# Optimization experiments

Measured on AMD Instinct MI355X. Metric: run time of the kernel, lower is better.

Reference implementation:

```python
import jax, jax.numpy as jnp
import numpy as np

B, C, H, W = 4, 256, 96, 96
PARA, MOD, NH = 256, 256, 128
PI = 3.14159  # constant used in the torch source (not math.pi)


def setup_inputs():
    key = jax.random.key(0)
    ks = jax.random.split(key, 16)
    w = lambda k, shp: jax.random.normal(k, shp, jnp.float32) * 0.02
    z = lambda n: jnp.zeros((n,), jnp.float32)
    return {
        "feature_map": jax.random.normal(ks[0], (B, C, H, W), jnp.float32),
        "para_code": jax.random.normal(ks[1], (B, PARA), jnp.float32),
        "style_code": jax.random.normal(ks[2], (B, MOD), jnp.float32),
        "lin_common_w": w(ks[3], (PARA, PARA)), "lin_common_b": z(PARA),
        "lin_scale_w": w(ks[4], (PARA, C)), "lin_scale_b": z(C),
        "lin_rot_w": w(ks[5], (PARA, C)), "lin_rot_b": z(C),
        "lin_trans_w": w(ks[6], (PARA, 2 * C)), "lin_trans_b": z(2 * C),
        "a1_shared_w": w(ks[7], (MOD, NH)), "a1_shared_b": z(NH),
        "a1_gamma_w": w(ks[8], (NH, C)), "a1_gamma_b": z(C),
        "a1_beta_w": w(ks[9], (NH, C)), "a1_beta_b": z(C),
        "conv1_w": w(ks[10], (C, C, 3, 3)), "conv1_b": z(C),
        "a2_shared_w": w(ks[11], (MOD, NH)), "a2_shared_b": z(NH),
        "a2_gamma_w": w(ks[12], (NH, C)), "a2_gamma_b": z(C),
        "a2_beta_w": w(ks[13], (NH, C)), "a2_beta_b": z(C),
        "conv2_w": w(ks[14], (C, C, 3, 3)), "conv2_b": z(C),
    }


def _adaat(fm, pc, cw, cb, sw, sb, rw, rb, tw, tb):
    # fm: [B,C,H,W]; per-channel 2D affine warp, channels act as depth of a 3D grid_sample.
    Bn, Cn, Hn, Wn = fm.shape
    pc = jax.nn.relu(pc @ cw + cb)
    scale = jax.nn.sigmoid(pc @ sw + sb) * 2.0            # [B,C]
    angle = jnp.tanh(pc @ rw + rb) * PI                   # [B,C]
    trans = jnp.tanh(pc @ tw + tb).reshape(Bn, Cn, 2)     # [B,C,2]
    cos = jnp.cos(angle)[:, :, None, None]
    sin = jnp.sin(angle)[:, :, None, None]
    sc = scale[:, :, None, None]
    tx = trans[:, :, 0][:, :, None, None]
    ty = trans[:, :, 1][:, :, None, None]
    # align_corners=True style normalized source grid (as in make_coordinate_grid_3d)
    gx = (2.0 * jnp.arange(Wn) / (Wn - 1) - 1.0)[None, :]  # [1,W]
    gy = (2.0 * jnp.arange(Hn) / (Hn - 1) - 1.0)[:, None]  # [H,1]
    # rotation [[cos,-sin],[sin,cos]] @ [x,y], then scale + translate -> [B,C,H,W]
    xw = (cos * gx - sin * gy) * sc + tx
    yw = (sin * gx + cos * gy) * sc + ty
    gz = 2.0 * jnp.arange(Cn) / (Cn - 1) - 1.0             # [C]
    # unnormalize with align_corners=False (torch grid_sample default)
    ix = ((xw + 1.0) * Wn - 1.0) * 0.5
    iy = ((yw + 1.0) * Hn - 1.0) * 0.5
    iz = (((gz + 1.0) * Cn - 1.0) * 0.5)[None, :, None, None]  # [1,C,1,1]
    x0 = jnp.floor(ix); y0 = jnp.floor(iy); z0 = jnp.floor(iz)
    wx = ix - x0; wy = iy - y0; wz = iz - z0
    x0 = x0.astype(jnp.int32); y0 = y0.astype(jnp.int32); z0 = z0.astype(jnp.int32)
    bidx = jnp.arange(Bn)[:, None, None, None]

    def gather(zi, yi, xi):
        valid = (zi >= 0) & (zi < Cn) & (yi >= 0) & (yi < Hn) & (xi >= 0) & (xi < Wn)
        v = fm[bidx, jnp.clip(zi, 0, Cn - 1), jnp.clip(yi, 0, Hn - 1), jnp.clip(xi, 0, Wn - 1)]
        return jnp.where(valid, v, 0.0)

    out = jnp.zeros_like(fm)
    for dz, wzc in ((0, 1.0 - wz), (1, wz)):
        for dy, wyc in ((0, 1.0 - wy), (1, wy)):
            for dx, wxc in ((0, 1.0 - wx), (1, wx)):
                out = out + gather(z0 + dz, y0 + dy, x0 + dx) * (wzc * wyc * wxc)
    return out


def _adain_layer(x, style, shw, shb, gw, gb, bw, bb):
    m = x.mean(axis=(2, 3), keepdims=True)
    v = x.var(axis=(2, 3), keepdims=True)  # biased, as torch InstanceNorm2d
    xn = (x - m) / jnp.sqrt(v + 1e-5)
    a = jax.nn.relu(style @ shw + shb)
    gamma = (a @ gw + gb)[:, :, None, None]
    beta = (a @ bw + bb)[:, :, None, None]
    return xn * (1.0 + gamma) + beta


def _conv3(x, w, b):
    y = jax.lax.conv_general_dilated(x, w, (1, 1), ((1, 1), (1, 1)),
                                     dimension_numbers=("NCHW", "OIHW", "NCHW"))
    return y + b[None, :, None, None]


def _lrelu(x):
    return jnp.where(x >= 0, x, 0.2 * x)


def reference(feature_map, para_code, style_code,
              lin_common_w, lin_common_b, lin_scale_w, lin_scale_b,
              lin_rot_w, lin_rot_b, lin_trans_w, lin_trans_b,
              a1_shared_w, a1_shared_b, a1_gamma_w, a1_gamma_b, a1_beta_w, a1_beta_b,
              conv1_w, conv1_b,
              a2_shared_w, a2_shared_b, a2_gamma_w, a2_gamma_b, a2_beta_w, a2_beta_b,
              conv2_w, conv2_b):
    t = _adaat(feature_map, para_code, lin_common_w, lin_common_b,
               lin_scale_w, lin_scale_b, lin_rot_w, lin_rot_b, lin_trans_w, lin_trans_b)
    x = _adain_layer(t, style_code, a1_shared_w, a1_shared_b, a1_gamma_w, a1_gamma_b, a1_beta_w, a1_beta_b)
    x = _conv3(_lrelu(x), conv1_w, conv1_b)
    x = _adain_layer(x, style_code, a2_shared_w, a2_shared_b, a2_gamma_w, a2_gamma_b, a2_beta_w, a2_beta_b)
    x = _conv3(_lrelu(x), conv2_w, conv2_b)
    return x
```

## Files before the change

### kernel.cpp

```cpp
#include <hip/hip_runtime.h>
#include <hip/hip_bf16.h>
#include <cstddef>

#define BATCH 4
#define CH 256
#define HH 96
#define WW 96
#define HWN (HH*WW)
#define NTOT (BATCH*CH*HWN)
#define XT_H 98
#define XT_W 98
#define XT_PLANE (XT_H*XT_W*CH)

typedef __attribute__((ext_vector_type(16))) float f32x16;
typedef __attribute__((ext_vector_type(8))) __bf16 bfrag;
typedef __attribute__((ext_vector_type(8))) unsigned short u16x8;

static __device__ __forceinline__ unsigned short f2bf(float f) {
  unsigned int u = __float_as_uint(f);
  unsigned int r = (u + 0x7fffu + ((u >> 16) & 1u)) >> 16;
  return (unsigned short)r;
}

__global__ __launch_bounds__(256) void params_kernel(
    const float* __restrict__ para, const float* __restrict__ style,
    const float* __restrict__ cw,  const float* __restrict__ cb,
    const float* __restrict__ sw,  const float* __restrict__ sb,
    const float* __restrict__ rw,  const float* __restrict__ rb,
    const float* __restrict__ tw,  const float* __restrict__ tb,
    const float* __restrict__ a1w, const float* __restrict__ a1b,
    const float* __restrict__ g1w, const float* __restrict__ g1b,
    const float* __restrict__ b1w, const float* __restrict__ b1b,
    const float* __restrict__ a2w, const float* __restrict__ a2b,
    const float* __restrict__ g2w, const float* __restrict__ g2b,
    const float* __restrict__ b2w, const float* __restrict__ b2b,
    float* __restrict__ warp, float* __restrict__ gb1, float* __restrict__ gb2)
{
  __shared__ float s_para[256], s_sty[256], s_pc[256], s_a1[128], s_a2[128];
  int b = blockIdx.x;
  int t = threadIdx.x;
  s_para[t] = para[b*256 + t];
  s_sty[t]  = style[b*256 + t];
  __syncthreads();

  float acc = cb[t];
  for (int i = 0; i < 256; i++) acc = fmaf(s_para[i], cw[i*256 + t], acc);
  s_pc[t] = fmaxf(acc, 0.f);

  if (t < 128) {
    float a = a1b[t];
    for (int i = 0; i < 256; i++) a = fmaf(s_sty[i], a1w[i*128 + t], a);
    s_a1[t] = fmaxf(a, 0.f);
  } else {
    int u = t - 128;
    float a = a2b[u];
    for (int i = 0; i < 256; i++) a = fmaf(s_sty[i], a2w[i*128 + u], a);
    s_a2[u] = fmaxf(a, 0.f);
  }
  __syncthreads();

  int c = t;
  float ds = sb[c], dr = rb[c], dtx = tb[2*c], dty = tb[2*c + 1];
  for (int i = 0; i < 256; i++) {
    float p = s_pc[i];
    ds  = fmaf(p, sw[i*256 + c], ds);
    dr  = fmaf(p, rw[i*256 + c], dr);
    dtx = fmaf(p, tw[i*512 + 2*c], dtx);
    dty = fmaf(p, tw[i*512 + 2*c + 1], dty);
  }
  float scale = 2.f / (1.f + expf(-ds));
  float ang = tanhf(dr) * 3.14159f;
  float sn, cs;
  sincosf(ang, &sn, &cs);
  int bc = b*256 + c;
  warp[bc*4 + 0] = cs * scale;
  warp[bc*4 + 1] = sn * scale;
  warp[bc*4 + 2] = tanhf(dtx);
  warp[bc*4 + 3] = tanhf(dty);

  float g1 = g1b[c], be1 = b1b[c], g2 = g2b[c], be2 = b2b[c];
  for (int i = 0; i < 128; i++) {
    float a = s_a1[i];
    g1  = fmaf(a, g1w[i*256 + c], g1);
    be1 = fmaf(a, b1w[i*256 + c], be1);
  }
  for (int i = 0; i < 128; i++) {
    float a = s_a2[i];
    g2  = fmaf(a, g2w[i*256 + c], g2);
    be2 = fmaf(a, b2w[i*256 + c], be2);
  }
  gb1[bc*2] = g1; gb1[bc*2 + 1] = be1;
  gb2[bc*2] = g2; gb2[bc*2 + 1] = be2;
}

__global__ __launch_bounds__(256) void prep_weights_kernel(
    const float* __restrict__ w1, const float* __restrict__ w2,
    unsigned short* __restrict__ wf1, unsigned short* __restrict__ wf2)
{
  int co = blockIdx.x & 255;
  const float* src = (blockIdx.x < 256) ? w1 : w2;
  unsigned short* dst = (blockIdx.x < 256) ? wf1 : wf2;
  int ci = threadIdx.x;
  int coblk = co >> 6, m = (co >> 5) & 1;
  int l = (co & 31) | (((ci >> 3) & 1) << 5);
  int ks = ci >> 4, j = ci & 7;
  const float* p = src + ((size_t)co * 256 + ci) * 9;
  #pragma unroll
  for (int tap = 0; tap < 9; tap++) {
    size_t idx = (((size_t)((coblk * 16 + ks) * 9 + tap) * 2 + m) * 64 + l) * 8 + j;
    dst[idx] = f2bf(p[tap]);
  }
}

__global__ __launch_bounds__(256) void adaat_kernel(
    const float* __restrict__ fm, const float* __restrict__ warp,
    const float* __restrict__ gb1, float* __restrict__ tout,
    float* __restrict__ nrm1)
{
  __shared__ float s[96 * 100];
  int bc = blockIdx.x;
  int b = bc >> 8, c = bc & 255;
  float csc = warp[bc*4 + 0], ssc = warp[bc*4 + 1];
  float tx = warp[bc*4 + 2], ty = warp[bc*4 + 3];

  const float axw = csc * (96.f / 95.f);
  const float axh = -ssc * (96.f / 95.f);
  const float ax0 = 48.f * (tx - csc + ssc) + 47.5f;
  const float ayw = ssc * (96.f / 95.f);
  const float ayh = csc * (96.f / 95.f);
  const float ay0 = 48.f * (ty - ssc - csc) + 47.5f;

  float iz = 256.f * (float)c / 255.f - 0.5f;
  float z0f = floorf(iz);
  float wz = iz - z0f;
  int z0 = (int)z0f;
  const float* p0 = (z0 >= 0) ? fm + (size_t)(b*256 + z0) * HWN : nullptr;
  const float* p1 = (z0 + 1 < 256) ? fm + (size_t)(b*256 + z0 + 1) * HWN : nullptr;
  float w0 = 1.f - wz, w1 = wz;

  int t = threadIdx.x;
  const float4* q0 = (const float4*)p0;
  const float4* q1 = (const float4*)p1;
  for (int i = t; i < 2304; i += 256) {
    int row = i / 24, col = i - row * 24;
    float4 r = {0.f, 0.f, 0.f, 0.f};
    if (q0) {
      float4 v = q0[i];
      r.x = w0 * v.x; r.y = w0 * v.y; r.z = w0 * v.z; r.w = w0 * v.w;
    }
    if (q1) {
      float4 v = q1[i];
      r.x = fmaf(w1, v.x, r.x); r.y = fmaf(w1, v.y, r.y);
      r.z = fmaf(w1, v.z, r.z); r.w = fmaf(w1, v.w, r.w);
    }
    *(float4*)&s[row * 100 + col * 4] = r;
  }
  __syncthreads();

  int h = t / 96, w = t - (t / 96) * 96;
  float* dst = tout + (size_t)bc * HWN;
  float sum = 0.f, sumsq = 0.f;
  #pragma unroll
  for (int k = 0; k < 36; k++) {
    float ix = fmaf(axw, (float)w, fmaf(axh, (float)h, ax0));
    float iy = fmaf(ayw, (float)w, fmaf(ayh, (float)h, ay0));
    float x0f = floorf(ix), y0f = floorf(iy);
    float wx = ix - x0f, wy = iy - y0f;
    int x0 = (int)x0f, y0 = (int)y0f;
    int x0c = min(max(x0, 0), 95), x1c = min(max(x0 + 1, 0), 95);
    int y0c = min(max(y0, 0), 95), y1c = min(max(y0 + 1, 0), 95);
    bool vx0 = (unsigned)x0 < 96u, vx1 = (unsigned)(x0 + 1) < 96u;
    bool vy0 = (unsigned)y0 < 96u, vy1 = (unsigned)(y0 + 1) < 96u;
    float a00 = s[y0c * 100 + x0c], a01 = s[y0c * 100 + x1c];
    float a10 = s[y1c * 100 + x0c], a11 = s[y1c * 100 + x1c];
    float wxm = 1.f - wx, wym = 1.f - wy;
    float w00 = (vy0 && vx0) ? wym * wxm : 0.f;
    float w01 = (vy0 && vx1) ? wym * wx  : 0.f;
    float w10 = (vy1 && vx0) ? wy * wxm  : 0.f;
    float w11 = (vy1 && vx1) ? wy * wx   : 0.f;
    float v = w00 * a00;
    v = fmaf(w01, a01, v);
    v = fmaf(w10, a10, v);
    v = fmaf(w11, a11, v);
    dst[t + k * 256] = v;
    sum += v;
    sumsq = fmaf(v, v, sumsq);
    int wn = w + 64;
    int carry = (wn >= 96) ? 1 : 0;
    w = wn - (carry ? 96 : 0);
    h += 2 + carry;
  }

  for (int off = 32; off > 0; off >>= 1) {
    sum   += __shfl_down(sum, off, 64);
    sumsq += __shfl_down(sumsq, off, 64);
  }
  __shared__ float rs[4], rq[4];
  int lane = t & 63, wvi = t >> 6;
  if (lane == 0) { rs[wvi] = sum; rq[wvi] = sumsq; }
  __syncthreads();
  if (t == 0) {
    float S = rs[0] + rs[1] + rs[2] + rs[3];
    float Q = rq[0] + rq[1] + rq[2] + rq[3];
    float m = S * (1.f / 9216.f);
    float var = Q * (1.f / 9216.f) - m * m;
    float rstd = rsqrtf(var + 1e-5f);
    float sc = (1.f + gb1[bc*2]) * rstd;
    nrm1[bc*2] = sc;
    nrm1[bc*2 + 1] = gb1[bc*2 + 1] - m * sc;
  }
}

__global__ __launch_bounds__(256) void stats_kernel(
    const float* __restrict__ x, const float* __restrict__ gb,
    float* __restrict__ nrm)
{
  int bc = blockIdx.x;
  const float4* p = (const float4*)(x + (size_t)bc * HWN);
  float sum = 0.f, sumsq = 0.f;
  for (int i = threadIdx.x; i < HWN / 4; i += 256) {
    float4 v = p[i];
    sum   += v.x + v.y + v.z + v.w;
    sumsq += v.x*v.x + v.y*v.y + v.z*v.z + v.w*v.w;
  }
  for (int off = 32; off > 0; off >>= 1) {
    sum   += __shfl_down(sum, off, 64);
    sumsq += __shfl_down(sumsq, off, 64);
  }
  __shared__ float rs[4], rq[4];
  int lane = threadIdx.x & 63, wv = threadIdx.x >> 6;
  if (lane == 0) { rs[wv] = sum; rq[wv] = sumsq; }
  __syncthreads();
  if (threadIdx.x == 0) {
    float S = rs[0] + rs[1] + rs[2] + rs[3];
    float Q = rq[0] + rq[1] + rq[2] + rq[3];
    float m = S * (1.f / 9216.f);
    float var = Q * (1.f / 9216.f) - m * m;
    float rstd = rsqrtf(var + 1e-5f);
    float sc = (1.f + gb[bc*2]) * rstd;
    nrm[bc*2] = sc;
    nrm[bc*2 + 1] = gb[bc*2 + 1] - m * sc;
  }
}

__global__ __launch_bounds__(256) void transpose_norm_kernel(
    const float* __restrict__ x, const float* __restrict__ nrm,
    unsigned short* __restrict__ xt)
{
  int hi = blockIdx.x;
  int b  = blockIdx.y;
  unsigned short* dst = xt + (size_t)b * XT_PLANE + (size_t)hi * (XT_W * CH);
  int t = threadIdx.x;
  int h = hi - 1;
  u16x8 zero = {0,0,0,0,0,0,0,0};
  if (h < 0 || h >= 96) {
    for (int c = t; c < XT_W * CH / 8; c += 256) ((u16x8*)dst)[c] = zero;
    return;
  }
  __shared__ unsigned short s[96 * 256];
  int ci = t;
  float sc = nrm[(b*256 + ci)*2], bi = nrm[(b*256 + ci)*2 + 1];
  const float* src = x + ((size_t)(b*256 + ci)) * HWN + h * 96;
  for (int wg = 0; wg < 24; wg++) {
    float4 v = *(const float4*)(src + wg * 4);
    float y0 = fmaf(v.x, sc, bi); y0 = (y0 >= 0.f) ? y0 : 0.2f * y0;
    float y1 = fmaf(v.y, sc, bi); y1 = (y1 >= 0.f) ? y1 : 0.2f * y1;
    float y2 = fmaf(v.z, sc, bi); y2 = (y2 >= 0.f) ? y2 : 0.2f * y2;
    float y3 = fmaf(v.w, sc, bi); y3 = (y3 >= 0.f) ? y3 : 0.2f * y3;
    s[(wg*4 + 0) * 256 + ci] = f2bf(y0);
    s[(wg*4 + 1) * 256 + ci] = f2bf(y1);
    s[(wg*4 + 2) * 256 + ci] = f2bf(y2);
    s[(wg*4 + 3) * 256 + ci] = f2bf(y3);
  }
  __syncthreads();
  for (int c = t; c < 98 * 32; c += 256) {
    int w = c >> 5, p = c & 31;
    u16x8 v = zero;
    if (w >= 1 && w <= 96) v = *(const u16x8*)&s[(w - 1) * 256 + p * 8];
    ((u16x8*)dst)[c] = v;
  }
}

__global__ __launch_bounds__(256, 3) void conv_mfma_kernel(
    const unsigned short* __restrict__ xt,
    const unsigned short* __restrict__ wf,
    const float* __restrict__ cb,
    float* __restrict__ out)
{
  __shared__ __align__(16) unsigned short s_in[2][784 * 8];

  int hb = blockIdx.x, coblk = blockIdx.y, b = blockIdx.z;
  int co0 = coblk * 64, h0 = hb * 2;
  int t = threadIdx.x, lane = t & 63, wv = t >> 6;
  int rw = wv >> 1, mh = wv & 1;
  int l31 = lane & 31, lhi = lane >> 5;
  const unsigned short* xtb = xt + (size_t)b * XT_PLANE;

  int pre_g[4];
  #pragma unroll
  for (int i = 0; i < 4; i++) {
    int c = t + i * 256;
    if (c < 784) {
      int r = c / 196;
      int rem = c - r * 196;
      int half = rem / 98;
      int w = rem - half * 98;
      pre_g[i] = ((h0 + r) * 98 + w) * 256 + half * 8;
    }
  }

  f32x16 acc[3];
  #pragma unroll
  for (int n = 0; n < 3; n++)
    #pragma unroll
    for (int i = 0; i < 16; i++) acc[n][i] = 0.f;

  const unsigned short* wfb = wf + (size_t)(coblk * 16) * 9216 + mh * 512 + lane * 8;

  u16x8 stg[4];
  #pragma unroll
  for (int i = 0; i < 3; i++) stg[i] = *(const u16x8*)(xtb + pre_g[i]);
  if (t < 16) stg[3] = *(const u16x8*)(xtb + pre_g[3]);
  #pragma unroll
  for (int i = 0; i < 3; i++) *(u16x8*)(&s_in[0][(t + i * 256) * 8]) = stg[i];
  if (t < 16) *(u16x8*)(&s_in[0][(t + 3 * 256) * 8]) = stg[3];

  bfrag wa[9];
  #pragma unroll
  for (int tap = 0; tap < 9; tap++) wa[tap] = *(const bfrag*)(wfb + tap * 1024);

  #pragma unroll
  for (int i = 0; i < 3; i++) stg[i] = *(const u16x8*)(xtb + pre_g[i] + 16);
  if (t < 16) stg[3] = *(const u16x8*)(xtb + pre_g[3] + 16);
  __syncthreads();

  int buf = 0;
  #pragma unroll 1
  for (int ks = 0; ks < 16; ks++) {
    const unsigned short* sb = s_in[buf];
    int ksn = (ks < 15) ? (ks + 1) : 15;
    const unsigned short* wkn = wfb + (size_t)ksn * 9216;
    #pragma unroll
    for (int ky = 0; ky < 3; ky++) {
      const unsigned short* srow = sb + (((rw + ky) * 2 + lhi) * 98) * 8;
      bfrag bb[9];
      #pragma unroll
      for (int kx = 0; kx < 3; kx++)
        #pragma unroll
        for (int n = 0; n < 3; n++)
          bb[kx * 3 + n] = *(const bfrag*)(srow + (n * 32 + kx + l31) * 8);
      #pragma unroll
      for (int kx = 0; kx < 3; kx++) {
        int tap = ky * 3 + kx;
        acc[0] = __builtin_amdgcn_mfma_f32_32x32x16_bf16(wa[tap], bb[kx*3+0], acc[0], 0, 0, 0);
        acc[1] = __builtin_amdgcn_mfma_f32_32x32x16_bf16(wa[tap], bb[kx*3+1], acc[1], 0, 0, 0);
        acc[2] = __builtin_amdgcn_mfma_f32_32x32x16_bf16(wa[tap], bb[kx*3+2], acc[2], 0, 0, 0);
        wa[tap] = *(const bfrag*)(wkn + tap * 1024);
      }
    }
    if (ks < 15) {
      unsigned short* sn = s_in[buf ^ 1];
      #pragma unroll
      for (int i = 0; i < 3; i++) *(u16x8*)(&sn[(t + i * 256) * 8]) = stg[i];
      if (t < 16) *(u16x8*)(&sn[(t + 3 * 256) * 8]) = stg[3];
      if (ks < 14) {
        int off = (ks + 2) * 16;
        #pragma unroll
        for (int i = 0; i < 3; i++) stg[i] = *(const u16x8*)(xtb + pre_g[i] + off);
        if (t < 16) stg[3] = *(const u16x8*)(xtb + pre_g[3] + off);
      }
    }
    __syncthreads();
    buf ^= 1;
  }

  int h = h0 + rw;
  #pragma unroll
  for (int r = 0; r < 16; r++) {
    int row = (r & 3) + 8 * (r >> 2) + 4 * lhi;
    int co = co0 + mh * 32 + row;
    float bv = cb[co];
    size_t base = ((size_t)(b * 256 + co) * 96 + h) * 96;
    #pragma unroll
    for (int n = 0; n < 3; n++) {
      out[base + n * 32 + l31] = acc[n][r] + bv;
    }
  }
}

extern "C" void kernel_launch(void* const* d_in, const int* in_sizes, int n_in,
                              void* d_out, int out_size, void* d_ws, size_t ws_size,
                              hipStream_t stream)
{
  const float* fm    = (const float*)d_in[0];
  const float* para  = (const float*)d_in[1];
  const float* style = (const float*)d_in[2];
  const float* cw  = (const float*)d_in[3];
  const float* cb  = (const float*)d_in[4];
  const float* sw  = (const float*)d_in[5];
  const float* sb  = (const float*)d_in[6];
  const float* rw  = (const float*)d_in[7];
  const float* rb  = (const float*)d_in[8];
  const float* tw  = (const float*)d_in[9];
  const float* tb  = (const float*)d_in[10];
  const float* a1w = (const float*)d_in[11];
  const float* a1b = (const float*)d_in[12];
  const float* g1w = (const float*)d_in[13];
  const float* g1b = (const float*)d_in[14];
  const float* b1w = (const float*)d_in[15];
  const float* b1b = (const float*)d_in[16];
  const float* c1w = (const float*)d_in[17];
  const float* c1b = (const float*)d_in[18];
  const float* a2w = (const float*)d_in[19];
  const float* a2b = (const float*)d_in[20];
  const float* g2w = (const float*)d_in[21];
  const float* g2b = (const float*)d_in[22];
  const float* b2w = (const float*)d_in[23];
  const float* b2b = (const float*)d_in[24];
  const float* c2w = (const float*)d_in[25];
  const float* c2b = (const float*)d_in[26];

  float* outf = (float*)d_out;

  unsigned short* xtbuf = (unsigned short*)d_ws;
  unsigned short* wf1   = xtbuf + (size_t)BATCH * XT_PLANE;
  unsigned short* wf2   = wf1 + 9 * 256 * 256;
  float* fws  = (float*)(wf2 + 9 * 256 * 256);
  float* warp = fws;
  float* gb1  = warp + 4 * 1024;
  float* gb2  = gb1 + 2 * 1024;
  float* nrm1 = gb2 + 2 * 1024;
  float* nrm2 = nrm1 + 2 * 1024;

  params_kernel<<<4, 256, 0, stream>>>(para, style, cw, cb, sw, sb, rw, rb, tw, tb,
      a1w, a1b, g1w, g1b, b1w, b1b, a2w, a2b, g2w, g2b, b2w, b2b, warp, gb1, gb2);
  prep_weights_kernel<<<512, 256, 0, stream>>>(c1w, c2w, wf1, wf2);
  adaat_kernel<<<1024, 256, 0, stream>>>(fm, warp, gb1, outf, nrm1);
  transpose_norm_kernel<<<dim3(98, 4), 256, 0, stream>>>(outf, nrm1, xtbuf);
  conv_mfma_kernel<<<dim3(48, 4, 4), 256, 0, stream>>>(xtbuf, wf1, c1b, outf);
  stats_kernel<<<1024, 256, 0, stream>>>(outf, gb2, nrm2);
  transpose_norm_kernel<<<dim3(98, 4), 256, 0, stream>>>(outf, nrm2, xtbuf);
  conv_mfma_kernel<<<dim3(48, 4, 4), 256, 0, stream>>>(xtbuf, wf2, c2b, outf);
}
```

Baseline: 221.3 us.

## Split parameter MLP kernel into two parallel stages with K-split reductions

```diff
diff --git a/kernel.cpp b/kernel.cpp
--- a/kernel.cpp
+++ b/kernel.cpp
@@ -22,75 +22,135 @@
   return (unsigned short)r;
 }
 
-__global__ __launch_bounds__(256) void params_kernel(
+__global__ __launch_bounds__(256) void params_stage1_kernel(
     const float* __restrict__ para, const float* __restrict__ style,
     const float* __restrict__ cw,  const float* __restrict__ cb,
+    const float* __restrict__ a1w, const float* __restrict__ a1b,
+    const float* __restrict__ a2w, const float* __restrict__ a2b,
+    float* __restrict__ pcbuf, float* __restrict__ a1buf, float* __restrict__ a2buf)
+{
+  __shared__ float s_in[256];
+  __shared__ float red[256];
+  int part = blockIdx.x, b = blockIdx.y, t = threadIdx.x;
+  s_in[t] = (part < 4) ? para[b*256 + t] : style[b*256 + t];
+  __syncthreads();
+  if (part < 4) {
+    int o = t & 63, ks = t >> 6, co0 = part * 64;
+    const float* wcol = cw + co0 + o;
+    float acc = 0.f;
+    #pragma unroll 8
+    for (int i = 0; i < 64; i++) {
+      int k = ks * 64 + i;
+      acc = fmaf(s_in[k], wcol[k * 256], acc);
+    }
+    red[t] = acc;
+    __syncthreads();
+    if (t < 64) {
+      float s = red[t] + red[t + 64] + red[t + 128] + red[t + 192];
+      pcbuf[b*256 + co0 + t] = fmaxf(s + cb[co0 + t], 0.f);
+    }
+  } else {
+    const float* w  = (part == 4) ? a1w : a2w;
+    const float* bb = (part == 4) ? a1b : a2b;
+    float* outp = (part == 4) ? a1buf : a2buf;
+    int o = t & 127, ks = t >> 7;
+    const float* wcol = w + o;
+    float acc = 0.f;
+    #pragma unroll 8
+    for (int i = 0; i < 128; i++) {
+      int k = ks * 128 + i;
+      acc = fmaf(s_in[k], wcol[k * 128], acc);
+    }
+    red[t] = acc;
+    __syncthreads();
+    if (t < 128) {
+      float s = red[t] + red[t + 128];
+      outp[b*128 + t] = fmaxf(s + bb[t], 0.f);
+    }
+  }
+}
+
+__global__ __launch_bounds__(256) void params_stage2_kernel(
+    const float* __restrict__ pcbuf, const float* __restrict__ a1buf,
+    const float* __restrict__ a2buf,
     const float* __restrict__ sw,  const float* __restrict__ sb,
     const float* __restrict__ rw,  const float* __restrict__ rb,
     const float* __restrict__ tw,  const float* __restrict__ tb,
-    const float* __restrict__ a1w, const float* __restrict__ a1b,
     const float* __restrict__ g1w, const float* __restrict__ g1b,
     const float* __restrict__ b1w, const float* __restrict__ b1b,
-    const float* __restrict__ a2w, const float* __restrict__ a2b,
     const float* __restrict__ g2w, const float* __restrict__ g2b,
     const float* __restrict__ b2w, const float* __restrict__ b2b,
     float* __restrict__ warp, float* __restrict__ gb1, float* __restrict__ gb2)
 {
-  __shared__ float s_para[256], s_sty[256], s_pc[256], s_a1[128], s_a2[128];
-  int b = blockIdx.x;
-  int t = threadIdx.x;
-  s_para[t] = para[b*256 + t];
-  s_sty[t]  = style[b*256 + t];
-  __syncthreads();
-
-  float acc = cb[t];
-  for (int i = 0; i < 256; i++) acc = fmaf(s_para[i], cw[i*256 + t], acc);
-  s_pc[t] = fmaxf(acc, 0.f);
-
-  if (t < 128) {
-    float a = a1b[t];
-    for (int i = 0; i < 256; i++) a = fmaf(s_sty[i], a1w[i*128 + t], a);
-    s_a1[t] = fmaxf(a, 0.f);
-  } else {
-    int u = t - 128;
-    float a = a2b[u];
-    for (int i = 0; i < 256; i++) a = fmaf(s_sty[i], a2w[i*128 + u], a);
-    s_a2[u] = fmaxf(a, 0.f);
-  }
-  __syncthreads();
-
-  int c = t;
-  float ds = sb[c], dr = rb[c], dtx = tb[2*c], dty = tb[2*c + 1];
-  for (int i = 0; i < 256; i++) {
+  __shared__ float s_pc[256], s_a1[128], s_a2[128];
+  __shared__ float red[8][4][16];
+  int co0 = blockIdx.x * 16, b = blockIdx.y, t = threadIdx.x;
+  s_pc[t] = pcbuf[b*256 + t];
+  if (t < 128) s_a1[t] = a1buf[b*128 + t];
+  else         s_a2[t - 128] = a2buf[b*128 + (t - 128)];
+  __syncthreads();
+
+  int cl = t & 15, klane = t >> 4;
+  int c = co0 + cl;
+  const float2* tw2 = (const float2*)tw;
+  float ds = 0.f, dr = 0.f, dtx = 0.f, dty = 0.f;
+  float g1 = 0.f, be1 = 0.f, g2 = 0.f, be2 = 0.f;
+  #pragma unroll 4
+  for (int kk = 0; kk < 16; kk++) {
+    int i = klane * 16 + kk;
     float p = s_pc[i];
     ds  = fmaf(p, sw[i*256 + c], ds);
     dr  = fmaf(p, rw[i*256 + c], dr);
-    dtx = fmaf(p, tw[i*512 + 2*c], dtx);
-    dty = fmaf(p, tw[i*512 + 2*c + 1], dty);
-  }
-  float scale = 2.f / (1.f + expf(-ds));
-  float ang = tanhf(dr) * 3.14159f;
-  float sn, cs;
-  sincosf(ang, &sn, &cs);
-  int bc = b*256 + c;
-  warp[bc*4 + 0] = cs * scale;
-  warp[bc*4 + 1] = sn * scale;
-  warp[bc*4 + 2] = tanhf(dtx);
-  warp[bc*4 + 3] = tanhf(dty);
-
-  float g1 = g1b[c], be1 = b1b[c], g2 = g2b[c], be2 = b2b[c];
-  for (int i = 0; i < 128; i++) {
+    float2 tv = tw2[i*256 + c];
+    dtx = fmaf(p, tv.x, dtx);
+    dty = fmaf(p, tv.y, dty);
+  }
+  #pragma unroll 4
+  for (int kk = 0; kk < 8; kk++) {
+    int i = klane * 8 + kk;
     float a = s_a1[i];
     g1  = fmaf(a, g1w[i*256 + c], g1);
     be1 = fmaf(a, b1w[i*256 + c], be1);
-  }
-  for (int i = 0; i < 128; i++) {
-    float a = s_a2[i];
-    g2  = fmaf(a, g2w[i*256 + c], g2);
-    be2 = fmaf(a, b2w[i*256 + c], be2);
-  }
-  gb1[bc*2] = g1; gb1[bc*2 + 1] = be1;
-  gb2[bc*2] = g2; gb2[bc*2 + 1] = be2;
+    float a2v = s_a2[i];
+    g2  = fmaf(a2v, g2w[i*256 + c], g2);
+    be2 = fmaf(a2v, b2w[i*256 + c], be2);
+  }
+  ds  += __shfl_down(ds, 32, 64);  ds  += __shfl_down(ds, 16, 64);
+  dr  += __shfl_down(dr, 32, 64);  dr  += __shfl_down(dr, 16, 64);
+  dtx += __shfl_down(dtx, 32, 64); dtx += __shfl_down(dtx, 16, 64);
+  dty += __shfl_down(dty, 32, 64); dty += __shfl_down(dty, 16, 64);
+  g1  += __shfl_down(g1, 32, 64);  g1  += __shfl_down(g1, 16, 64);
+  be1 += __shfl_down(be1, 32, 64); be1 += __shfl_down(be1, 16, 64);
+  g2  += __shfl_down(g2, 32, 64);  g2  += __shfl_down(g2, 16, 64);
+  be2 += __shfl_down(be2, 32, 64); be2 += __shfl_down(be2, 16, 64);
+  int wv = t >> 6;
+  if ((t & 63) < 16) {
+    red[0][wv][cl] = ds;  red[1][wv][cl] = dr;
+    red[2][wv][cl] = dtx; red[3][wv][cl] = dty;
+    red[4][wv][cl] = g1;  red[5][wv][cl] = be1;
+    red[6][wv][cl] = g2;  red[7][wv][cl] = be2;
+  }
+  __syncthreads();
+  if (t < 16) {
+    float v[8];
+    #pragma unroll
+    for (int o = 0; o < 8; o++)
+      v[o] = red[o][0][t] + red[o][1][t] + red[o][2][t] + red[o][3][t];
+    int cc = co0 + t;
+    int bc = b*256 + cc;
+    float scale = 2.f / (1.f + expf(-(v[0] + sb[cc])));
+    float ang = tanhf(v[1] + rb[cc]) * 3.14159f;
+    float sn, cs;
+    sincosf(ang, &sn, &cs);
+    warp[bc*4 + 0] = cs * scale;
+    warp[bc*4 + 1] = sn * scale;
+    warp[bc*4 + 2] = tanhf(v[2] + tb[2*cc]);
+    warp[bc*4 + 3] = tanhf(v[3] + tb[2*cc + 1]);
+    gb1[bc*2]     = v[4] + g1b[cc];
+    gb1[bc*2 + 1] = v[5] + b1b[cc];
+    gb2[bc*2]     = v[6] + g2b[cc];
+    gb2[bc*2 + 1] = v[7] + b2b[cc];
+  }
 }
 
 __global__ __launch_bounds__(256) void prep_weights_kernel(
@@ -431,9 +491,15 @@
   float* gb2  = gb1 + 2 * 1024;
   float* nrm1 = gb2 + 2 * 1024;
   float* nrm2 = nrm1 + 2 * 1024;
-
-  params_kernel<<<4, 256, 0, stream>>>(para, style, cw, cb, sw, sb, rw, rb, tw, tb,
-      a1w, a1b, g1w, g1b, b1w, b1b, a2w, a2b, g2w, g2b, b2w, b2b, warp, gb1, gb2);
+  float* pcbuf = nrm2 + 2 * 1024;
+  float* a1buf = pcbuf + 1024;
+  float* a2buf = a1buf + 512;
+
+  params_stage1_kernel<<<dim3(6, 4), 256, 0, stream>>>(para, style, cw, cb,
+      a1w, a1b, a2w, a2b, pcbuf, a1buf, a2buf);
+  params_stage2_kernel<<<dim3(16, 4), 256, 0, stream>>>(pcbuf, a1buf, a2buf,
+      sw, sb, rw, rb, tw, tb, g1w, g1b, b1w, b1b, g2w, g2b, b2w, b2b,
+      warp, gb1, gb2);
   prep_weights_kernel<<<512, 256, 0, stream>>>(c1w, c2w, wf1, wf2);
   adaat_kernel<<<1024, 256, 0, stream>>>(fm, warp, gb1, outf, nrm1);
   transpose_norm_kernel<<<dim3(98, 4), 256, 0, stream>>>(outf, nrm1, xtbuf);
```

Result: faster. 191.3 us (-13.6%).
